# Performance work log

Measured on AMD Instinct MI355X. Metric: run time of the kernel, lower is better.

The kernel has to match this reference:

```python
import jax, jax.numpy as jnp
import numpy as np

L, B, D_IN, D_H = 512, 128, 256, 512

def setup_inputs() -> dict:
    key = jax.random.key(0)
    k1, k2, k3, k4, k5 = jax.random.split(key, 5)
    s_x = 1.0 / np.sqrt(D_IN)
    s_h = 1.0 / np.sqrt(D_H)
    return {
        "x": jax.random.normal(k1, (L, B, D_IN), dtype=jnp.float32),
        "h0": jnp.zeros((B, D_H), dtype=jnp.float32),
        "Wx": jax.random.uniform(k2, (D_IN, D_H), minval=-s_x, maxval=s_x, dtype=jnp.float32),
        "bx": jax.random.uniform(k3, (D_H,), minval=-s_x, maxval=s_x, dtype=jnp.float32),
        "Wh": jax.random.uniform(k4, (D_H, D_H), minval=-s_h, maxval=s_h, dtype=jnp.float32),
        "bh": jax.random.uniform(k5, (D_H,), minval=-s_h, maxval=s_h, dtype=jnp.float32),
    }

def reference(x, h0, Wx, bx, Wh, bh):
    # Batch the input projection across all timesteps upfront: [L, B, D_H]
    xp = jnp.einsum('lbi,ih->lbh', x, Wx) + bx

    def step(h, xp_t):
        h = jnp.tanh(xp_t + h @ Wh + bh)
        return h, h

    _, hs = jax.lax.scan(step, h0, xp)
    return hs  # [L, B, D_H] -- stacked hidden states, as torch.stack(results)
```

## Files before the change

### kernel.cpp

```cpp
#include <hip/hip_runtime.h>
#include <stdint.h>

typedef __fp16 half2v __attribute__((ext_vector_type(2)));
typedef __fp16 half8v __attribute__((ext_vector_type(8)));
typedef float floatx4 __attribute__((ext_vector_type(4)));

#define Lr   512
#define Br   128
#define DINr 256
#define DHr  512

__device__ __forceinline__ float fdot2(half2v a, half2v b, float c) {
    return __builtin_amdgcn_fdot2(a, b, c, false);
}
__device__ __forceinline__ uint32_t pk_u32(float lo, float hi) {
    half2v h = __builtin_amdgcn_cvt_pkrtz(lo, hi);
    return __builtin_bit_cast(uint32_t, h);
}
__device__ __forceinline__ half2v u32_h2(uint32_t u) {
    return __builtin_bit_cast(half2v, u);
}

__global__ __launch_bounds__(512)
void wxcvt_kernel(const float* __restrict__ Wx, __fp16* __restrict__ bt)
{
    const int gid = blockIdx.x * 512 + threadIdx.x;
    const int k = gid >> 9;
    const int n = gid & 511;
    const int s = k >> 5, g = (k >> 3) & 3, j = k & 7;
    const int nt = n >> 4, r = n & 15;
    const int idx = ((((nt * 8 + s) * 4 + g) * 16 + r) * 8) + j;
    bt[idx] = (__fp16)Wx[gid];
}

__global__ __launch_bounds__(512)
void xp_mfma_kernel(const float* __restrict__ x, const __fp16* __restrict__ bt,
                    const float* __restrict__ bx, float* __restrict__ out)
{
    const int tid  = threadIdx.x;
    const int w    = tid >> 6;
    const int lane = tid & 63;
    const int g    = lane >> 4;
    const int r    = lane & 15;
    const int m0   = blockIdx.x * 128 + w * 16;

    const float* xrow = x + (size_t)(m0 + r) * DINr;
    half8v af[8];
    #pragma unroll
    for (int s = 0; s < 8; ++s) {
        const float4 u = *(const float4*)(xrow + 32 * s + 8 * g);
        const float4 v = *(const float4*)(xrow + 32 * s + 8 * g + 4);
        half8v a;
        a[0] = (__fp16)u.x; a[1] = (__fp16)u.y; a[2] = (__fp16)u.z; a[3] = (__fp16)u.w;
        a[4] = (__fp16)v.x; a[5] = (__fp16)v.y; a[6] = (__fp16)v.z; a[7] = (__fp16)v.w;
        af[s] = a;
    }

    const half8v* bt8 = (const half8v*)bt;

    #pragma unroll 4
    for (int nt = 0; nt < 32; ++nt) {
        floatx4 acc = {0.f, 0.f, 0.f, 0.f};
        #pragma unroll
        for (int s = 0; s < 8; ++s) {
            const half8v bf = bt8[((nt * 8 + s) * 4 + g) * 16 + r];
            acc = __builtin_amdgcn_mfma_f32_16x16x32_f16(af[s], bf, acc, 0, 0, 0);
        }
        const float bxv = bx[nt * 16 + r];
        #pragma unroll
        for (int q = 0; q < 4; ++q) {
            out[(size_t)(m0 + 4 * g + q) * DHr + nt * 16 + r] = acc[q] + bxv;
        }
    }
}

__global__ __launch_bounds__(512)
void rnn_kernel(const float* __restrict__ h0, const float* __restrict__ Wh,
                const float* __restrict__ bh, float* __restrict__ out)
{
    const int tid   = threadIdx.x;
    const int b     = blockIdx.x;
    const int lane  = tid & 63;
    const int wv    = tid >> 6;
    const int p     = wv * 32 + (lane & 31);
    const int s     = lane >> 5;
    const int mycol = (lane < 32) ? p : (p + 256);

    __shared__ __align__(16) uint32_t hbuf[2][256];
    __shared__ __align__(16) uint4 wldsA2[8][512];
    __shared__ __align__(16) uint4 wldsB2[8][512];

    half2v wr0[96], wr1[96];
    #pragma unroll
    for (int q = 0; q < 96; ++q) {
        const int k = 2 * (s * 128 + q);
        const float* Wk  = Wh + (size_t)k * DHr;
        const float* Wk1 = Wk + DHr;
        wr0[q] = __builtin_amdgcn_cvt_pkrtz(Wk[p],       Wk1[p]);
        wr1[q] = __builtin_amdgcn_cvt_pkrtz(Wk[p + 256], Wk1[p + 256]);
    }
    #pragma unroll
    for (int c = 0; c < 8; ++c) {
        uint4 qa, qb;
        uint32_t* qaw = (uint32_t*)&qa;
        uint32_t* qbw = (uint32_t*)&qb;
        #pragma unroll
        for (int j = 0; j < 4; ++j) {
            const int q = 96 + 4 * c + j;
            const int k = 2 * (s * 128 + q);
            const float* Wk  = Wh + (size_t)k * DHr;
            const float* Wk1 = Wk + DHr;
            qaw[j] = pk_u32(Wk[p],       Wk1[p]);
            qbw[j] = pk_u32(Wk[p + 256], Wk1[p + 256]);
        }
        wldsA2[c][tid] = qa;
        wldsB2[c][tid] = qb;
    }
    const float bhv = bh[mycol];
    float xpv = out[(size_t)b * DHr + mycol];

    if (tid < 256) {
        const float* h0b = h0 + (size_t)b * DHr + 2 * tid;
        hbuf[0][tid] = pk_u32(h0b[0], h0b[1]);
    }
    __syncthreads();

    #pragma unroll 1
    for (int t = 0; t < Lr; ++t) {
        const uint32_t* hb = &hbuf[t & 1][s * 128];
        float ac00 = 0.f, ac01 = 0.f, ac10 = 0.f, ac11 = 0.f;
        #pragma unroll
        for (int c = 0; c < 24; ++c) {
            const uint4 hv = *(const uint4*)&hb[c * 4];
            ac00 = fdot2(u32_h2(hv.x), wr0[4*c+0], ac00);
            ac10 = fdot2(u32_h2(hv.x), wr1[4*c+0], ac10);
            ac01 = fdot2(u32_h2(hv.y), wr0[4*c+1], ac01);
            ac11 = fdot2(u32_h2(hv.y), wr1[4*c+1], ac11);
            ac00 = fdot2(u32_h2(hv.z), wr0[4*c+2], ac00);
            ac10 = fdot2(u32_h2(hv.z), wr1[4*c+2], ac10);
            ac01 = fdot2(u32_h2(hv.w), wr0[4*c+3], ac01);
            ac11 = fdot2(u32_h2(hv.w), wr1[4*c+3], ac11);
        }
        #pragma unroll
        for (int c = 0; c < 8; ++c) {
            const uint4 hv = *(const uint4*)&hb[96 + c * 4];
            const uint4 wa = wldsA2[c][tid];
            const uint4 wb = wldsB2[c][tid];
            ac00 = fdot2(u32_h2(hv.x), u32_h2(wa.x), ac00);
            ac10 = fdot2(u32_h2(hv.x), u32_h2(wb.x), ac10);
            ac01 = fdot2(u32_h2(hv.y), u32_h2(wa.y), ac01);
            ac11 = fdot2(u32_h2(hv.y), u32_h2(wb.y), ac11);
            ac00 = fdot2(u32_h2(hv.z), u32_h2(wa.z), ac00);
            ac10 = fdot2(u32_h2(hv.z), u32_h2(wb.z), ac10);
            ac01 = fdot2(u32_h2(hv.w), u32_h2(wa.w), ac01);
            ac11 = fdot2(u32_h2(hv.w), u32_h2(wb.w), ac11);
        }
        const float sA = ac00 + ac01;
        const float sB = ac10 + ac11;
        const float rA = sA + __shfl_xor(sA, 32, 64);
        const float rB = sB + __shfl_xor(sB, 32, 64);
        const float sum = (lane < 32) ? rA : rB;

        const float svv = sum + xpv + bhv;
        const float e   = __expf(2.f * svv);
        const float h   = 1.f - 2.f * __builtin_amdgcn_rcpf(e + 1.f);

        out[(size_t)(t * Br + b) * DHr + mycol] = h;
        if (t + 1 < Lr)
            xpv = out[(size_t)((t + 1) * Br + b) * DHr + mycol];

        const float hx = __shfl_xor(h, 1, 64);
        if (!(lane & 1))
            hbuf[(t + 1) & 1][mycol >> 1] = pk_u32(h, hx);
        __syncthreads();
    }
}

extern "C" void kernel_launch(void* const* d_in, const int* in_sizes, int n_in,
                              void* d_out, int out_size, void* d_ws, size_t ws_size,
                              hipStream_t stream) {
    (void)in_sizes; (void)n_in; (void)ws_size; (void)out_size;
    const float* x  = (const float*)d_in[0];
    const float* h0 = (const float*)d_in[1];
    const float* Wx = (const float*)d_in[2];
    const float* bx = (const float*)d_in[3];
    const float* Wh = (const float*)d_in[4];
    const float* bh = (const float*)d_in[5];
    float* out  = (float*)d_out;
    __fp16* bt  = (__fp16*)d_ws;

    wxcvt_kernel<<<dim3(256), dim3(512), 0, stream>>>(Wx, bt);
    xp_mfma_kernel<<<dim3(512), dim3(512), 0, stream>>>(x, bt, bx, out);
    rnn_kernel<<<dim3(128), dim3(512), 0, stream>>>(h0, Wh, bh, out);
}
```

Measured before the change: 994.7 us.

## Split RNN reduction by K-half across waves and broadcast h via readlane

Reorganizes the recurrent step so each wave handles one K-half for 128 contiguous output columns, with h values broadcast to all lanes through readlane from a single per-lane LDS load instead of repeated vector LDS reads. The cross-half partial sums now go through a shared-memory array and an extra barrier per step rather than a wave shuffle, and the h buffer is single-buffered. This aims to cut LDS read traffic in the inner loop, but adds a second __syncthreads per timestep and many scalar readlane operations.

```diff
diff --git a/kernel.cpp b/kernel.cpp
--- a/kernel.cpp
+++ b/kernel.cpp
@@ -78,26 +78,29 @@
 void rnn_kernel(const float* __restrict__ h0, const float* __restrict__ Wh,
                 const float* __restrict__ bh, float* __restrict__ out)
 {
-    const int tid   = threadIdx.x;
-    const int b     = blockIdx.x;
-    const int lane  = tid & 63;
-    const int wv    = tid >> 6;
-    const int p     = wv * 32 + (lane & 31);
-    const int s     = lane >> 5;
-    const int mycol = (lane < 32) ? p : (p + 256);
-
-    __shared__ __align__(16) uint32_t hbuf[2][256];
+    const int tid  = threadIdx.x;
+    const int b    = blockIdx.x;
+    const int lane = tid & 63;
+    const int wv   = tid >> 6;
+    const int kh   = wv >> 2;
+    const int cg   = wv & 3;
+    const int c0   = cg * 128 + lane;
+    const int c1   = c0 + 64;
+    const int myc  = kh ? c1 : c0;
+
+    __shared__ __align__(8)  uint32_t hbuf[256];
+    __shared__ float part[512];
     __shared__ __align__(16) uint4 wldsA2[8][512];
     __shared__ __align__(16) uint4 wldsB2[8][512];
 
     half2v wr0[96], wr1[96];
     #pragma unroll
     for (int q = 0; q < 96; ++q) {
-        const int k = 2 * (s * 128 + q);
+        const int k = 2 * (kh * 128 + q);
         const float* Wk  = Wh + (size_t)k * DHr;
         const float* Wk1 = Wk + DHr;
-        wr0[q] = __builtin_amdgcn_cvt_pkrtz(Wk[p],       Wk1[p]);
-        wr1[q] = __builtin_amdgcn_cvt_pkrtz(Wk[p + 256], Wk1[p + 256]);
+        wr0[q] = __builtin_amdgcn_cvt_pkrtz(Wk[c0], Wk1[c0]);
+        wr1[q] = __builtin_amdgcn_cvt_pkrtz(Wk[c1], Wk1[c1]);
     }
     #pragma unroll
     for (int c = 0; c < 8; ++c) {
@@ -105,73 +108,77 @@
         uint32_t* qaw = (uint32_t*)&qa;
         uint32_t* qbw = (uint32_t*)&qb;
         #pragma unroll
-        for (int j = 0; j < 4; ++j) {
-            const int q = 96 + 4 * c + j;
-            const int k = 2 * (s * 128 + q);
+        for (int jj = 0; jj < 4; ++jj) {
+            const int q = 96 + 4 * c + jj;
+            const int k = 2 * (kh * 128 + q);
             const float* Wk  = Wh + (size_t)k * DHr;
             const float* Wk1 = Wk + DHr;
-            qaw[j] = pk_u32(Wk[p],       Wk1[p]);
-            qbw[j] = pk_u32(Wk[p + 256], Wk1[p + 256]);
+            qaw[jj] = pk_u32(Wk[c0], Wk1[c0]);
+            qbw[jj] = pk_u32(Wk[c1], Wk1[c1]);
         }
         wldsA2[c][tid] = qa;
         wldsB2[c][tid] = qb;
     }
-    const float bhv = bh[mycol];
-    float xpv = out[(size_t)b * DHr + mycol];
+
+    const float bhv = bh[myc];
+    float xpv = out[(size_t)b * DHr + myc];
 
     if (tid < 256) {
         const float* h0b = h0 + (size_t)b * DHr + 2 * tid;
-        hbuf[0][tid] = pk_u32(h0b[0], h0b[1]);
+        hbuf[tid] = pk_u32(h0b[0], h0b[1]);
     }
     __syncthreads();
 
     #pragma unroll 1
     for (int t = 0; t < Lr; ++t) {
-        const uint32_t* hb = &hbuf[t & 1][s * 128];
-        float ac00 = 0.f, ac01 = 0.f, ac10 = 0.f, ac11 = 0.f;
-        #pragma unroll
-        for (int c = 0; c < 24; ++c) {
-            const uint4 hv = *(const uint4*)&hb[c * 4];
-            ac00 = fdot2(u32_h2(hv.x), wr0[4*c+0], ac00);
-            ac10 = fdot2(u32_h2(hv.x), wr1[4*c+0], ac10);
-            ac01 = fdot2(u32_h2(hv.y), wr0[4*c+1], ac01);
-            ac11 = fdot2(u32_h2(hv.y), wr1[4*c+1], ac11);
-            ac00 = fdot2(u32_h2(hv.z), wr0[4*c+2], ac00);
-            ac10 = fdot2(u32_h2(hv.z), wr1[4*c+2], ac10);
-            ac01 = fdot2(u32_h2(hv.w), wr0[4*c+3], ac01);
-            ac11 = fdot2(u32_h2(hv.w), wr1[4*c+3], ac11);
+        const uint2 hp = *(const uint2*)&hbuf[kh * 128 + 2 * lane];
+
+        float a0e = 0.f, a0o = 0.f, a1e = 0.f, a1o = 0.f;
+        #pragma unroll
+        for (int m = 0; m < 48; ++m) {
+            const uint32_t se = __builtin_amdgcn_readlane(hp.x, m);
+            const uint32_t so = __builtin_amdgcn_readlane(hp.y, m);
+            a0e = fdot2(u32_h2(se), wr0[2*m],   a0e);
+            a1e = fdot2(u32_h2(se), wr1[2*m],   a1e);
+            a0o = fdot2(u32_h2(so), wr0[2*m+1], a0o);
+            a1o = fdot2(u32_h2(so), wr1[2*m+1], a1o);
         }
         #pragma unroll
         for (int c = 0; c < 8; ++c) {
-            const uint4 hv = *(const uint4*)&hb[96 + c * 4];
             const uint4 wa = wldsA2[c][tid];
             const uint4 wb = wldsB2[c][tid];
-            ac00 = fdot2(u32_h2(hv.x), u32_h2(wa.x), ac00);
-            ac10 = fdot2(u32_h2(hv.x), u32_h2(wb.x), ac10);
-            ac01 = fdot2(u32_h2(hv.y), u32_h2(wa.y), ac01);
-            ac11 = fdot2(u32_h2(hv.y), u32_h2(wb.y), ac11);
-            ac00 = fdot2(u32_h2(hv.z), u32_h2(wa.z), ac00);
-            ac10 = fdot2(u32_h2(hv.z), u32_h2(wb.z), ac10);
-            ac01 = fdot2(u32_h2(hv.w), u32_h2(wa.w), ac01);
-            ac11 = fdot2(u32_h2(hv.w), u32_h2(wb.w), ac11);
-        }
-        const float sA = ac00 + ac01;
-        const float sB = ac10 + ac11;
-        const float rA = sA + __shfl_xor(sA, 32, 64);
-        const float rB = sB + __shfl_xor(sB, 32, 64);
-        const float sum = (lane < 32) ? rA : rB;
-
-        const float svv = sum + xpv + bhv;
-        const float e   = __expf(2.f * svv);
-        const float h   = 1.f - 2.f * __builtin_amdgcn_rcpf(e + 1.f);
-
-        out[(size_t)(t * Br + b) * DHr + mycol] = h;
+            const int m0 = 48 + 2 * c;
+            const uint32_t se0 = __builtin_amdgcn_readlane(hp.x, m0);
+            const uint32_t so0 = __builtin_amdgcn_readlane(hp.y, m0);
+            const uint32_t se1 = __builtin_amdgcn_readlane(hp.x, m0 + 1);
+            const uint32_t so1 = __builtin_amdgcn_readlane(hp.y, m0 + 1);
+            a0e = fdot2(u32_h2(se0), u32_h2(wa.x), a0e);
+            a1e = fdot2(u32_h2(se0), u32_h2(wb.x), a1e);
+            a0o = fdot2(u32_h2(so0), u32_h2(wa.y), a0o);
+            a1o = fdot2(u32_h2(so0), u32_h2(wb.y), a1o);
+            a0e = fdot2(u32_h2(se1), u32_h2(wa.z), a0e);
+            a1e = fdot2(u32_h2(se1), u32_h2(wb.z), a1e);
+            a0o = fdot2(u32_h2(so1), u32_h2(wa.w), a0o);
+            a1o = fdot2(u32_h2(so1), u32_h2(wb.w), a1o);
+        }
+        const float s0 = a0e + a0o;
+        const float s1 = a1e + a1o;
+
+        part[kh ? c0 : c1] = kh ? s0 : s1;
+        __syncthreads();
+
+        const float sown = kh ? s1 : s0;
+        const float o    = sown + part[myc] + xpv + bhv;
+        const float e    = __expf(2.f * o);
+        const float h    = 1.f - 2.f * __builtin_amdgcn_rcpf(e + 1.f);
+
+        out[(size_t)(t * Br + b) * DHr + myc] = h;
         if (t + 1 < Lr)
-            xpv = out[(size_t)((t + 1) * Br + b) * DHr + mycol];
-
-        const float hx = __shfl_xor(h, 1, 64);
+            xpv = out[(size_t)((t + 1) * Br + b) * DHr + myc];
+
+        const float hn = __shfl_xor(h, 1, 64);
         if (!(lane & 1))
-            hbuf[(t + 1) & 1][mycol >> 1] = pk_u32(h, hx);
+            hbuf[cg * 64 + kh * 32 + (lane >> 1)] = pk_u32(h, hn);
         __syncthreads();
     }
 }
```

Result: slower. 1.218 ms (+22.4%).
